# Kernel optimization log

Hardware: AMD Instinct MI355X
Metric: run time of the kernel (lower is better)

Reference implementation:

```python
import jax, jax.numpy as jnp
import numpy as np

D = 1024      # input_dim
H = 4096      # hidden_dim
E = 8         # expert_count
TOP_K = 2
N = 8192      # tokens
LN_EPS = 1e-5


def setup_inputs() -> dict:
    key = jax.random.key(0)
    ks = jax.random.split(key, 10)
    s_d = 1.0 / np.sqrt(D)
    s_h = 1.0 / np.sqrt(H)
    return {
        "x": jax.random.normal(ks[0], (N, D), dtype=jnp.float32),
        "ln_gamma": jnp.ones((D,), jnp.float32),
        "ln_beta": jnp.zeros((D,), jnp.float32),
        "conf_w": jax.random.uniform(ks[1], (D, 1), jnp.float32, -s_d, s_d),
        "conf_b": jnp.zeros((1,), jnp.float32),
        "router_w": jax.random.uniform(ks[2], (D, E), jnp.float32, -s_d, s_d),
        "router_b": jnp.zeros((E,), jnp.float32),
        "w1": jax.random.uniform(ks[3], (E, D, H), jnp.float32, -s_d, s_d),
        "b1": jax.random.uniform(ks[4], (E, H), jnp.float32, -s_d, s_d),
        "w2": jax.random.uniform(ks[5], (E, H, D), jnp.float32, -s_h, s_h),
        "b2": jax.random.uniform(ks[6], (E, D), jnp.float32, -s_h, s_h),
    }


def reference(x, ln_gamma, ln_beta, conf_w, conf_b, router_w, router_b, w1, b1, w2, b2):
    # LayerNorm (torch default eps=1e-5, affine)
    mu = jnp.mean(x, axis=-1, keepdims=True)
    var = jnp.mean(jnp.square(x - mu), axis=-1, keepdims=True)
    x_norm = (x - mu) * jax.lax.rsqrt(var + LN_EPS) * ln_gamma + ln_beta

    # layer-skip confidence head
    confidence = jax.nn.sigmoid(x_norm @ conf_w + conf_b)  # [N,1]

    # router: softmax -> top-k -> renormalize selected weights
    router_probs = jax.nn.softmax(x_norm @ router_w + router_b, axis=-1)  # [N,E]
    vals, indices = jax.lax.top_k(router_probs, TOP_K)                    # [N,K]
    vals = vals / jnp.sum(vals, axis=-1, keepdims=True)

    # scatter top-k weights into dense per-expert combine weights [N,E]
    combine_w = jnp.zeros((x.shape[0], E), x.dtype).at[
        jnp.arange(x.shape[0])[:, None], indices].add(vals)

    # dispatch/combine: loop over small fixed expert count (dense compute,
    # weighted by combine_w, mathematically identical to per-token dispatch)
    combined = jnp.zeros_like(x)
    for e in range(E):
        h = jax.nn.relu(x_norm @ w1[e] + b1[e])      # [N,H]
        combined = combined + combine_w[:, e:e + 1] * (h @ w2[e] + b2[e])

    output = x + combined
    return output, confidence, x
```

## Files before the change

kernel.cpp:

```cpp
#include <hip/hip_runtime.h>
#include <hip/hip_bf16.h>

#define N_TOK 8192
#define DIM   1024
#define HID   4096
#define NEXP  8
#define CSTR  64
#define RTMAX 136
#define HROWS 16896
#define EPS   264
#define NG1   (8 * 2 * RTMAX)

using bf16x8 = __attribute__((ext_vector_type(8))) short;
using f32x4  = __attribute__((ext_vector_type(4))) float;

__device__ __forceinline__ void gload_lds16(const void* g, void* l) {
  __builtin_amdgcn_global_load_lds(
      (const __attribute__((address_space(1))) unsigned int*)g,
      (__attribute__((address_space(3))) unsigned int*)l, 16, 0, 0);
}

__device__ __forceinline__ float wredsum(float v) {
#pragma unroll
  for (int off = 32; off > 0; off >>= 1) v += __shfl_xor(v, off, 64);
  return v;
}

__device__ __forceinline__ unsigned short f2bf(float f) {
  __hip_bfloat16 h = __float2bfloat16(f);
  return *reinterpret_cast<unsigned short*>(&h);
}
__device__ __forceinline__ float bf2f(unsigned short u) {
  return __uint_as_float((unsigned)u << 16);
}

__device__ __forceinline__ void transpose_body(
    const float* __restrict__ src, __hip_bfloat16* __restrict__ dst,
    int R, int C, int c0, int r0, float (*tile)[65]) {
  const int tid = threadIdx.x;
  const int tx = tid & 15, ty = tid >> 4;
#pragma unroll
  for (int k = 0; k < 4; k++) {
    const int row = ty + k * 16;
    const float4 v = *(const float4*)(src + (size_t)(r0 + row) * C + c0 + tx * 4);
    tile[row][tx * 4 + 0] = v.x; tile[row][tx * 4 + 1] = v.y;
    tile[row][tx * 4 + 2] = v.z; tile[row][tx * 4 + 3] = v.w;
  }
  __syncthreads();
#pragma unroll
  for (int k = 0; k < 4; k++) {
    const int orow = ty + k * 16;
    ushort4 st;
    st.x = f2bf(tile[tx * 4 + 0][orow]);
    st.y = f2bf(tile[tx * 4 + 1][orow]);
    st.z = f2bf(tile[tx * 4 + 2][orow]);
    st.w = f2bf(tile[tx * 4 + 3][orow]);
    *(ushort4*)((unsigned short*)dst + (size_t)(c0 + orow) * R + r0 + tx * 4) = st;
  }
}

__global__ __launch_bounds__(256) void setup_kernel(
    const float* __restrict__ x, const float* __restrict__ gamma, const float* __restrict__ beta,
    const float* __restrict__ conf_w, const float* __restrict__ conf_b,
    const float* __restrict__ rw, const float* __restrict__ rb,
    const float* __restrict__ w1,
    __hip_bfloat16* __restrict__ w1t,
    __hip_bfloat16* __restrict__ xn, float* __restrict__ out,
    int* __restrict__ counts, int* __restrict__ lists, float* __restrict__ wts,
    int2* __restrict__ idx) {
  __shared__ float tile[64][65];
  const int b = (int)blockIdx.x;
  if (b < 8192) {
    const int z = b >> 10, r = b & 1023;
    const int cx = r & 63, ry = r >> 6;
    transpose_body(w1 + (size_t)z * DIM * HID, w1t + (size_t)z * DIM * HID,
                   DIM, HID, cx * 64, ry * 64, tile);
    return;
  }
  const int t = (b - 8192) * 4 + ((int)threadIdx.x >> 6);
  const int lane = threadIdx.x & 63;
  const float* xr = x + (size_t)t * DIM;

  float4 xv[4];
#pragma unroll
  for (int q = 0; q < 4; q++) xv[q] = *(const float4*)(xr + q * 256 + lane * 4);

  float s = 0.f, s2 = 0.f;
#pragma unroll
  for (int q = 0; q < 4; q++) {
    s  += xv[q].x + xv[q].y + xv[q].z + xv[q].w;
    s2 += xv[q].x * xv[q].x + xv[q].y * xv[q].y + xv[q].z * xv[q].z + xv[q].w * xv[q].w;
  }
  s = wredsum(s); s2 = wredsum(s2);
  const float mu  = s * (1.f / DIM);
  const float inv = rsqrtf(s2 * (1.f / DIM) - mu * mu + 1e-5f);

  float p[9];
#pragma unroll
  for (int e = 0; e < 9; e++) p[e] = 0.f;

#pragma unroll
  for (int q = 0; q < 4; q++) {
    const int d0 = q * 256 + lane * 4;
    const float4 g4 = *(const float4*)(gamma + d0);
    const float4 b4 = *(const float4*)(beta + d0);
    float v0 = (xv[q].x - mu) * inv * g4.x + b4.x;
    float v1 = (xv[q].y - mu) * inv * g4.y + b4.y;
    float v2 = (xv[q].z - mu) * inv * g4.z + b4.z;
    float v3 = (xv[q].w - mu) * inv * g4.w + b4.w;

    ushort4 st; st.x = f2bf(v0); st.y = f2bf(v1); st.z = f2bf(v2); st.w = f2bf(v3);
    *(ushort4*)((unsigned short*)xn + (size_t)t * DIM + d0) = st;
    *(float4*)(out + (size_t)N_TOK * DIM + N_TOK + (size_t)t * DIM + d0) = xv[q];

    const float vv[4] = {v0, v1, v2, v3};
#pragma unroll
    for (int j = 0; j < 4; j++) {
      const int d = d0 + j;
      const float v = vv[j];
      p[8] += v * conf_w[d];
      const float4 r0 = *(const float4*)(rw + d * 8);
      const float4 r1 = *(const float4*)(rw + d * 8 + 4);
      p[0] += v * r0.x; p[1] += v * r0.y; p[2] += v * r0.z; p[3] += v * r0.w;
      p[4] += v * r1.x; p[5] += v * r1.y; p[6] += v * r1.z; p[7] += v * r1.w;
    }
  }
#pragma unroll
  for (int e = 0; e < 9; e++) p[e] = wredsum(p[e]);

  if (lane == 0) {
    float L[8];
#pragma unroll
    for (int e = 0; e < 8; e++) L[e] = p[e] + rb[e];
    const float cl = p[8] + conf_b[0];
    out[(size_t)N_TOK * DIM + t] = 1.f / (1.f + expf(-cl));

    float mx = L[0];
#pragma unroll
    for (int e = 1; e < 8; e++) mx = fmaxf(mx, L[e]);
    float pe[8];
#pragma unroll
    for (int e = 0; e < 8; e++) pe[e] = expf(L[e] - mx);
    int i0 = 0; float v0 = pe[0];
#pragma unroll
    for (int e = 1; e < 8; e++) if (pe[e] > v0) { v0 = pe[e]; i0 = e; }
    int i1 = -1; float v1 = -1.f;
#pragma unroll
    for (int e = 0; e < 8; e++) if (e != i0 && pe[e] > v1) { v1 = pe[e]; i1 = e; }
    const float wsum = v0 + v1;
    const float w0 = v0 / wsum, w1v = v1 / wsum;
    int p0 = atomicAdd(&counts[i0 * CSTR], 1);
    lists[i0 * N_TOK + p0] = t; wts[i0 * N_TOK + p0] = w0;
    int p1 = atomicAdd(&counts[i1 * CSTR], 1);
    lists[i1 * N_TOK + p1] = t; wts[i1 * N_TOK + p1] = w1v;
    idx[t] = make_int2((i0 << 13) | p0, (i1 << 13) | p1);
  }
}

__global__ void bases_kernel(const int* __restrict__ counts, int* __restrict__ bases,
                             int* __restrict__ meta) {
  if (threadIdx.x == 0) {
    int s = 0, r = 0;
#pragma unroll
    for (int e = 0; e < NEXP; e++) {
      bases[e] = s; meta[e] = r;
      const int c = counts[e * CSTR];
      s += c; r += (c + 127) >> 7;
    }
    meta[NEXP] = r;
  }
}


#define LGKM_SB(N)                                                            \
  asm volatile("s_waitcnt lgkmcnt(" #N ")" ::: "memory");                     \
  __builtin_amdgcn_sched_barrier(0);

#define MFMA_G(MI)                                                            \
  __builtin_amdgcn_s_setprio(1);                                              \
  _Pragma("unroll")                                                           \
  for (int n = 0; n < 4; n++)                                                 \
    acc[MI][n] = __builtin_amdgcn_mfma_f32_16x16x32_bf16(afr[MI], bfr[n], acc[MI][n], 0, 0, 0); \
  __builtin_amdgcn_s_setprio(0);

#define GEMM_CORE(NT)                                                                   \
  f32x4 acc[8][4] = {};                                                                 \
  stage(0, 0); stage(1, 24576);                                                         \
  for (int t = 0; t < (NT); ++t) {                                                      \
    const int pb = (t % 3) * 24576;                                                     \
    if (t + 1 < (NT)) { asm volatile("s_waitcnt vmcnt(6)" ::: "memory"); }              \
    else              { asm volatile("s_waitcnt vmcnt(0)" ::: "memory"); }              \
    __builtin_amdgcn_s_barrier();                                                       \
    if (t + 2 < (NT)) stage(t + 2, ((t + 2) % 3) * 24576);                              \
    const char* Ab = smem + pb + Abase;                                                 \
    const char* Bb = smem + pb + Bbase;                                                 \
    bf16x8 bfr[4], afr[8];                                                              \
    afr[0] = *(const bf16x8*)(Ab);                                                      \
    bfr[0] = *(const bf16x8*)(Bb);                                                      \
    bfr[1] = *(const bf16x8*)(Bb + 1024);                                               \
    __builtin_amdgcn_sched_barrier(0);                                                  \
    bfr[2] = *(const bf16x8*)(Bb + 2048);                                               \
    bfr[3] = *(const bf16x8*)(Bb + 3072);                                               \
    __builtin_amdgcn_sched_barrier(0);                                                  \
    _Pragma("unroll")                                                                   \
    for (int m = 1; m < 8; m++) {                                                       \
      afr[m] = *(const bf16x8*)(Ab + m * 1024);                                         \
      __builtin_amdgcn_sched_barrier(0);                                                \
    }                                                                                   \
    LGKM_SB(7) MFMA_G(0)                                                                \
    LGKM_SB(6) MFMA_G(1)                                                                \
    LGKM_SB(5) MFMA_G(2)                                                                \
    LGKM_SB(4) MFMA_G(3)                                                                \
    LGKM_SB(3) MFMA_G(4)                                                                \
    LGKM_SB(2) MFMA_G(5)                                                                \
    LGKM_SB(1) MFMA_G(6)                                                                \
    LGKM_SB(0) MFMA_G(7)                                                                \
  }

#define DECODE_TAIL()                                                         \
  if (rtg >= meta[NEXP]) return;                                              \
  int e = 0;                                                                  \
  _Pragma("unroll")                                                           \
  for (int k = 1; k < NEXP; k++) if (meta[k] <= rtg) e = k;                   \
  const int rt = rtg - meta[e];                                               \
  const int cnt = counts[e * CSTR];                                           \
  const int hbase = bases[e];

#define GEMM_COMMON()                                                         \
  const int tid = threadIdx.x;                     \
  const int l = tid & 63;                                                     \
  const int wc = tid >> 6;                                                    \
  const int lr = l & 15;                                                      \
  const int pchunk = (l >> 4) ^ ((lr >> 1) & 3);                              \
  const int Abase = lr * 64 + pchunk * 16;                                    \
  const int Bbase = 8192 + (wc * 64 + lr) * 64 + pchunk * 16;                 \
  const int srow = tid >> 2;                       \
  const int lc = (tid & 3) ^ ((srow >> 1) & 3);

#define EPILOGUE(DSTROW)                                                      \
  __builtin_amdgcn_s_barrier();                                               \
  {                                                                           \
    unsigned short* ep = (unsigned short*)smem;                               \
    _Pragma("unroll")                                                         \
    for (int n = 0; n < 4; n++) {                                             \
      const int col = wc * 64 + n * 16 + lr;                                  \
      _Pragma("unroll")                                                       \
      for (int m = 0; m < 8; m++) {                                           \
        f32x4 v = acc[m][n];                                                  \
        _Pragma("unroll")                                                     \
        for (int j = 0; j < 4; j++) {                                         \
          const int row = m * 16 + (l >> 4) * 4 + j;                          \
          ep[row * EPS + col] = f2bf(v[j]);                                   \
        }                                                                     \
      }                                                                       \
    }                                                                         \
    asm volatile("s_waitcnt lgkmcnt(0)" ::: "memory");                        \
    __builtin_amdgcn_s_barrier();                                             \
    const int g = tid >> 5, u = tid & 31;                                     \
    _Pragma("unroll")                                                         \
    for (int i = 0; i < 16; i++) {                                            \
      const int row = i * 8 + g;                                              \
      const int pos = rt * 128 + row;                                         \
      if (pos < cnt) {                                                        \
        bf16x8 vv = *(const bf16x8*)(ep + row * EPS + u * 8);                 \
        *(bf16x8*)(DSTROW + u * 8) = vv;                                      \
      }                                                                       \
    }                                                                         \
  }

__global__ __launch_bounds__(256, 2) void gemm1_kernel(
    const __hip_bfloat16* __restrict__ xn, const __hip_bfloat16* __restrict__ w1t_b,
    const float* __restrict__ b1, const int* __restrict__ lists,
    const int* __restrict__ counts, const int* __restrict__ bases,
    const int* __restrict__ meta, __hip_bfloat16* __restrict__ hbuf,
    const float* __restrict__ w2, __hip_bfloat16* __restrict__ w2t) {
  __shared__ char smem[73728];
  if ((int)blockIdx.x >= NG1) {
    const int bb = (int)blockIdx.x - NG1;
    const int z = bb >> 10, r = bb & 1023;
    const int cx = r & 15, ry = r >> 4;
    transpose_body(w2 + (size_t)z * HID * DIM, w2t + (size_t)z * HID * DIM,
                   HID, DIM, cx * 64, ry * 64, (float(*)[65])smem);
    return;
  }
  const int x_ = (int)blockIdx.x & 7;
  const int q_ = (int)blockIdx.x >> 3;
  const int rtg = q_ >> 1;
  const int panel = x_ * 2 + (q_ & 1);
  DECODE_TAIL()
  const int ct = panel;
  const int* list = lists + e * N_TOK;
  const __hip_bfloat16* w1t = w1t_b + (size_t)e * DIM * HID;
  GEMM_COMMON()

  const int ap0 = rt * 128 + srow, ap1 = ap0 + 64;
  const int tok0 = list[ap0 < cnt ? ap0 : 0];
  const int tok1 = list[ap1 < cnt ? ap1 : 0];
  const unsigned short* srcA0 = (const unsigned short*)xn + (size_t)tok0 * DIM + lc * 8;
  const unsigned short* srcA1 = (const unsigned short*)xn + (size_t)tok1 * DIM + lc * 8;
  const unsigned short* srcB0 = (const unsigned short*)w1t + (size_t)(ct * 256 + srow) * DIM + lc * 8;
  const unsigned short* srcB1 = (const unsigned short*)w1t + (size_t)(ct * 256 + 64 + srow) * DIM + lc * 8;
  const unsigned short* srcB2 = (const unsigned short*)w1t + (size_t)(ct * 256 + 128 + srow) * DIM + lc * 8;
  const unsigned short* srcB3 = (const unsigned short*)w1t + (size_t)(ct * 256 + 192 + srow) * DIM + lc * 8;

  auto stage = [&](int tt, int lbase) {
    gload_lds16(srcA0 + tt * 32, smem + lbase + tid * 16);
    gload_lds16(srcA1 + tt * 32, smem + lbase + 4096 + tid * 16);
    gload_lds16(srcB0 + tt * 32, smem + lbase + 8192 + tid * 16);
    gload_lds16(srcB1 + tt * 32, smem + lbase + 12288 + tid * 16);
    gload_lds16(srcB2 + tt * 32, smem + lbase + 16384 + tid * 16);
    gload_lds16(srcB3 + tt * 32, smem + lbase + 20480 + tid * 16);
  };

  GEMM_CORE(DIM / 32)

  const float bv[4] = {
    b1[e * HID + ct * 256 + wc * 64 + 0 * 16 + lr],
    b1[e * HID + ct * 256 + wc * 64 + 1 * 16 + lr],
    b1[e * HID + ct * 256 + wc * 64 + 2 * 16 + lr],
    b1[e * HID + ct * 256 + wc * 64 + 3 * 16 + lr]};
#pragma unroll
  for (int n = 0; n < 4; n++)
#pragma unroll
    for (int m = 0; m < 8; m++)
#pragma unroll
      for (int j = 0; j < 4; j++) acc[m][n][j] = fmaxf(acc[m][n][j] + bv[n], 0.f);
  EPILOGUE((unsigned short*)hbuf + (size_t)(hbase + pos) * HID + ct * 256)
}

__global__ __launch_bounds__(256, 2) void gemm2_kernel(
    const __hip_bfloat16* __restrict__ hbuf, const __hip_bfloat16* __restrict__ w2t_b,
    const int* __restrict__ counts, const int* __restrict__ bases,
    const int* __restrict__ meta, __hip_bfloat16* __restrict__ ybuf, const int SK) {
  __shared__ char smem[73728];
  int panel, rtg;
  if (SK == 2) {
    const int x_ = (int)blockIdx.x & 7;
    const int q_ = (int)blockIdx.x >> 3;
    rtg = (q_ >> 2) * 4 + (x_ >> 1);
    panel = (x_ & 1) * 4 + (q_ & 3);
  } else {
    panel = (int)blockIdx.x / RTMAX;
    rtg = (int)blockIdx.x - panel * RTMAX;
  }
  DECODE_TAIL()
  const int ct = panel & 3;
  const int ksp = panel >> 2;
  const int kbase = ksp * (HID / SK);
  const __hip_bfloat16* w2t = w2t_b + (size_t)e * DIM * HID;
  GEMM_COMMON()

  const unsigned short* srcA0 = (const unsigned short*)hbuf +
      (size_t)(hbase + rt * 128 + srow) * HID + kbase + lc * 8;
  const unsigned short* srcA1 = (const unsigned short*)hbuf +
      (size_t)(hbase + rt * 128 + 64 + srow) * HID + kbase + lc * 8;
  const unsigned short* srcB0 = (const unsigned short*)w2t +
      (size_t)(ct * 256 + srow) * HID + kbase + lc * 8;
  const unsigned short* srcB1 = (const unsigned short*)w2t +
      (size_t)(ct * 256 + 64 + srow) * HID + kbase + lc * 8;
  const unsigned short* srcB2 = (const unsigned short*)w2t +
      (size_t)(ct * 256 + 128 + srow) * HID + kbase + lc * 8;
  const unsigned short* srcB3 = (const unsigned short*)w2t +
      (size_t)(ct * 256 + 192 + srow) * HID + kbase + lc * 8;

  auto stage = [&](int tt, int lbase) {
    gload_lds16(srcA0 + tt * 32, smem + lbase + tid * 16);
    gload_lds16(srcA1 + tt * 32, smem + lbase + 4096 + tid * 16);
    gload_lds16(srcB0 + tt * 32, smem + lbase + 8192 + tid * 16);
    gload_lds16(srcB1 + tt * 32, smem + lbase + 12288 + tid * 16);
    gload_lds16(srcB2 + tt * 32, smem + lbase + 16384 + tid * 16);
    gload_lds16(srcB3 + tt * 32, smem + lbase + 20480 + tid * 16);
  };

  const int nk = (HID / 32) / SK;
  GEMM_CORE(nk)

  EPILOGUE((unsigned short*)ybuf + ((size_t)ksp * HROWS + hbase + pos) * DIM + ct * 256)
}

__global__ __launch_bounds__(256) void combine_kernel(
    const float* __restrict__ x, const __hip_bfloat16* __restrict__ ybuf,
    const float* __restrict__ b2, const int2* __restrict__ idx,
    const float* __restrict__ wv, const int* __restrict__ bases,
    float* __restrict__ out, const int SK) {
  const int t = blockIdx.x * 4 + (threadIdx.x >> 6);
  const int lane = threadIdx.x & 63;
  const int2 iv = idx[t];
  const int e0 = iv.x >> 13, p0 = iv.x & (N_TOK - 1);
  const int e1 = iv.y >> 13, p1 = iv.y & (N_TOK - 1);
  const float w0 = wv[iv.x], w1 = wv[iv.y];
  const int r0 = bases[e0] + p0;
  const int r1 = bases[e1] + p1;
#pragma unroll
  for (int q = 0; q < 4; q++) {
    const int d0 = q * 256 + lane * 4;
    float4 o = *(const float4*)(x + (size_t)t * DIM + d0);
    float y0x = 0.f, y0y = 0.f, y0z = 0.f, y0w = 0.f;
    float y1x = 0.f, y1y = 0.f, y1z = 0.f, y1w = 0.f;
    for (int s = 0; s < SK; s++) {
      const ushort4 a = *(const ushort4*)((const unsigned short*)ybuf +
                          ((size_t)s * HROWS + r0) * DIM + d0);
      const ushort4 b = *(const ushort4*)((const unsigned short*)ybuf +
                          ((size_t)s * HROWS + r1) * DIM + d0);
      y0x += bf2f(a.x); y0y += bf2f(a.y); y0z += bf2f(a.z); y0w += bf2f(a.w);
      y1x += bf2f(b.x); y1y += bf2f(b.y); y1z += bf2f(b.z); y1w += bf2f(b.w);
    }
    const float4 bb0 = *(const float4*)(b2 + e0 * DIM + d0);
    const float4 bb1 = *(const float4*)(b2 + e1 * DIM + d0);
    o.x += w0 * (y0x + bb0.x) + w1 * (y1x + bb1.x);
    o.y += w0 * (y0y + bb0.y) + w1 * (y1y + bb1.y);
    o.z += w0 * (y0z + bb0.z) + w1 * (y1z + bb1.z);
    o.w += w0 * (y0w + bb0.w) + w1 * (y1w + bb1.w);
    *(float4*)(out + (size_t)t * DIM + d0) = o;
  }
}

extern "C" void kernel_launch(void* const* d_in, const int* in_sizes, int n_in,
                              void* d_out, int out_size, void* d_ws, size_t ws_size,
                              hipStream_t stream) {
  (void)in_sizes; (void)n_in; (void)out_size;
  const float* x      = (const float*)d_in[0];
  const float* gamma  = (const float*)d_in[1];
  const float* beta   = (const float*)d_in[2];
  const float* conf_w = (const float*)d_in[3];
  const float* conf_b = (const float*)d_in[4];
  const float* rw     = (const float*)d_in[5];
  const float* rb     = (const float*)d_in[6];
  const float* w1     = (const float*)d_in[7];
  const float* b1     = (const float*)d_in[8];
  const float* w2     = (const float*)d_in[9];
  const float* b2     = (const float*)d_in[10];
  float* out = (float*)d_out;

  char* w = (char*)d_ws;
  auto alloc = [&](size_t bytes) { char* p = w; w += (bytes + 255) & ~255ULL; return p; };

  __hip_bfloat16* xn = (__hip_bfloat16*)alloc((size_t)N_TOK * DIM * 2);
  int*   lists  = (int*)alloc((size_t)NEXP * N_TOK * 4);
  float* wtsb   = (float*)alloc((size_t)NEXP * N_TOK * 4);
  int*   counts = (int*)alloc(NEXP * CSTR * 4);
  int*   bases  = (int*)alloc(256);
  int*   meta   = (int*)alloc(256);
  int2*  idx    = (int2*)alloc((size_t)N_TOK * 8);

  const size_t hbufA = (size_t)HROWS * HID * 2;
  const size_t wtA   = (size_t)NEXP * DIM * HID * 2;
  __hip_bfloat16* hbuf = (__hip_bfloat16*)alloc(hbufA);
  __hip_bfloat16* w1t  = (__hip_bfloat16*)alloc(wtA);
  __hip_bfloat16* w2t  = (__hip_bfloat16*)alloc(wtA);
  const size_t used = (size_t)(w - (char*)d_ws);
  const size_t ybuf1 = (size_t)HROWS * DIM * 2;

  int SK;
  __hip_bfloat16* ybuf;
  if (ws_size >= used + 2 * ybuf1 + 4096) {
    SK = 2; ybuf = (__hip_bfloat16*)alloc(2 * ybuf1);
  } else {
    SK = 1; ybuf = w1t;
  }
  const int g2grid = (SK == 2) ? 8 * RTMAX : 4 * RTMAX;

  hipMemsetAsync(counts, 0, NEXP * CSTR * 4, stream);
  setup_kernel<<<8192 + N_TOK / 4, 256, 0, stream>>>(
      x, gamma, beta, conf_w, conf_b, rw, rb, w1, w1t,
      xn, out, counts, lists, wtsb, idx);
  bases_kernel<<<1, 64, 0, stream>>>(counts, bases, meta);
  gemm1_kernel<<<NG1 + 8192, 256, 0, stream>>>(xn, w1t, b1, lists, counts, bases, meta,
                                               hbuf, w2, w2t);
  gemm2_kernel<<<g2grid, 256, 0, stream>>>(hbuf, w2t, counts, bases, meta, ybuf, SK);
  combine_kernel<<<N_TOK / 4, 256, 0, stream>>>(x, ybuf, b2, idx, wtsb, bases, out, SK);
}
```

Baseline: 459.4 us.

## Load weight B-fragments directly into registers with one-step prefetch, bypassing LDS

Both expert GEMM kernels now stage only the activation (A) tiles through LDS. Each wave loads its own weight (B) fragments straight from global memory into registers, one K-step ahead. B tiles were never shared across waves, so this removes the LDS writes and reads for B and shrinks the triple-buffered LDS footprint to a third. The cost is that global-load latency for B is hidden by only one iteration of MFMA work. The register copy at the end of each loop forces a wait on those loads, and in-order vmcnt may also make it wait on the A prefetch, which can serialize memory and compute. It also raises register pressure.

```diff
diff --git a/kernel.cpp b/kernel.cpp
--- a/kernel.cpp
+++ b/kernel.cpp
@@ -180,30 +180,27 @@
   __builtin_amdgcn_s_setprio(1);                                              \
   _Pragma("unroll")                                                           \
   for (int n = 0; n < 4; n++)                                                 \
-    acc[MI][n] = __builtin_amdgcn_mfma_f32_16x16x32_bf16(afr[MI], bfr[n], acc[MI][n], 0, 0, 0); \
+    acc[MI][n] = __builtin_amdgcn_mfma_f32_16x16x32_bf16(afr[MI], bcur[n], acc[MI][n], 0, 0, 0); \
   __builtin_amdgcn_s_setprio(0);
 
 #define GEMM_CORE(NT)                                                                   \
   f32x4 acc[8][4] = {};                                                                 \
-  stage(0, 0); stage(1, 24576);                                                         \
+  bf16x8 bcur[4], bnxt[4];                                                              \
+  stageA(0, 0); stageA(1, 8192);                                                        \
+  loadB(0, bcur);                                                                       \
   for (int t = 0; t < (NT); ++t) {                                                      \
-    const int pb = (t % 3) * 24576;                                                     \
+    const int pb = (t % 3) * 8192;                                                      \
     if (t + 1 < (NT)) { asm volatile("s_waitcnt vmcnt(6)" ::: "memory"); }              \
-    else              { asm volatile("s_waitcnt vmcnt(0)" ::: "memory"); }              \
+    else              { asm volatile("s_waitcnt vmcnt(4)" ::: "memory"); }              \
     __builtin_amdgcn_s_barrier();                                                       \
-    if (t + 2 < (NT)) stage(t + 2, ((t + 2) % 3) * 24576);                              \
+    if (t + 1 < (NT)) loadB(t + 1, bnxt);                                               \
+    __builtin_amdgcn_sched_barrier(0);                                                  \
+    if (t + 2 < (NT)) stageA(t + 2, ((t + 2) % 3) * 8192);                              \
+    __builtin_amdgcn_sched_barrier(0);                                                  \
     const char* Ab = smem + pb + Abase;                                                 \
-    const char* Bb = smem + pb + Bbase;                                                 \
-    bf16x8 bfr[4], afr[8];                                                              \
-    afr[0] = *(const bf16x8*)(Ab);                                                      \
-    bfr[0] = *(const bf16x8*)(Bb);                                                      \
-    bfr[1] = *(const bf16x8*)(Bb + 1024);                                               \
-    __builtin_amdgcn_sched_barrier(0);                                                  \
-    bfr[2] = *(const bf16x8*)(Bb + 2048);                                               \
-    bfr[3] = *(const bf16x8*)(Bb + 3072);                                               \
-    __builtin_amdgcn_sched_barrier(0);                                                  \
+    bf16x8 afr[8];                                                                      \
     _Pragma("unroll")                                                                   \
-    for (int m = 1; m < 8; m++) {                                                       \
+    for (int m = 0; m < 8; m++) {                                                       \
       afr[m] = *(const bf16x8*)(Ab + m * 1024);                                         \
       __builtin_amdgcn_sched_barrier(0);                                                \
     }                                                                                   \
@@ -215,6 +212,9 @@
     LGKM_SB(2) MFMA_G(5)                                                                \
     LGKM_SB(1) MFMA_G(6)                                                                \
     LGKM_SB(0) MFMA_G(7)                                                                \
+    __builtin_amdgcn_sched_barrier(0);                                                  \
+    _Pragma("unroll")                                                                   \
+    for (int n = 0; n < 4; n++) bcur[n] = bnxt[n];                                      \
   }
 
 #define DECODE_TAIL()                                                         \
@@ -233,7 +233,6 @@
   const int lr = l & 15;                                                      \
   const int pchunk = (l >> 4) ^ ((lr >> 1) & 3);                              \
   const int Abase = lr * 64 + pchunk * 16;                                    \
-  const int Bbase = 8192 + (wc * 64 + lr) * 64 + pchunk * 16;                 \
   const int srow = tid >> 2;                       \
   const int lc = (tid & 3) ^ ((srow >> 1) & 3);
 
@@ -298,18 +297,17 @@
   const int tok1 = list[ap1 < cnt ? ap1 : 0];
   const unsigned short* srcA0 = (const unsigned short*)xn + (size_t)tok0 * DIM + lc * 8;
   const unsigned short* srcA1 = (const unsigned short*)xn + (size_t)tok1 * DIM + lc * 8;
-  const unsigned short* srcB0 = (const unsigned short*)w1t + (size_t)(ct * 256 + srow) * DIM + lc * 8;
-  const unsigned short* srcB1 = (const unsigned short*)w1t + (size_t)(ct * 256 + 64 + srow) * DIM + lc * 8;
-  const unsigned short* srcB2 = (const unsigned short*)w1t + (size_t)(ct * 256 + 128 + srow) * DIM + lc * 8;
-  const unsigned short* srcB3 = (const unsigned short*)w1t + (size_t)(ct * 256 + 192 + srow) * DIM + lc * 8;
-
-  auto stage = [&](int tt, int lbase) {
+  auto stageA = [&](int tt, int lbase) {
     gload_lds16(srcA0 + tt * 32, smem + lbase + tid * 16);
     gload_lds16(srcA1 + tt * 32, smem + lbase + 4096 + tid * 16);
-    gload_lds16(srcB0 + tt * 32, smem + lbase + 8192 + tid * 16);
-    gload_lds16(srcB1 + tt * 32, smem + lbase + 12288 + tid * 16);
-    gload_lds16(srcB2 + tt * 32, smem + lbase + 16384 + tid * 16);
-    gload_lds16(srcB3 + tt * 32, smem + lbase + 20480 + tid * 16);
+  };
+
+  const unsigned short* bptr = (const unsigned short*)w1t +
+      (size_t)(ct * 256 + wc * 64 + lr) * DIM + (l >> 4) * 8;
+  auto loadB = [&](int tt, bf16x8* dst) {
+#pragma unroll
+    for (int n = 0; n < 4; n++)
+      dst[n] = *(const bf16x8*)(bptr + (size_t)n * 16 * DIM + tt * 32);
   };
 
   GEMM_CORE(DIM / 32)
@@ -354,22 +352,17 @@
       (size_t)(hbase + rt * 128 + srow) * HID + kbase + lc * 8;
   const unsigned short* srcA1 = (const unsigned short*)hbuf +
       (size_t)(hbase + rt * 128 + 64 + srow) * HID + kbase + lc * 8;
-  const unsigned short* srcB0 = (const unsigned short*)w2t +
-      (size_t)(ct * 256 + srow) * HID + kbase + lc * 8;
-  const unsigned short* srcB1 = (const unsigned short*)w2t +
-      (size_t)(ct * 256 + 64 + srow) * HID + kbase + lc * 8;
-  const unsigned short* srcB2 = (const unsigned short*)w2t +
-      (size_t)(ct * 256 + 128 + srow) * HID + kbase + lc * 8;
-  const unsigned short* srcB3 = (const unsigned short*)w2t +
-      (size_t)(ct * 256 + 192 + srow) * HID + kbase + lc * 8;
-
-  auto stage = [&](int tt, int lbase) {
+  auto stageA = [&](int tt, int lbase) {
     gload_lds16(srcA0 + tt * 32, smem + lbase + tid * 16);
     gload_lds16(srcA1 + tt * 32, smem + lbase + 4096 + tid * 16);
-    gload_lds16(srcB0 + tt * 32, smem + lbase + 8192 + tid * 16);
-    gload_lds16(srcB1 + tt * 32, smem + lbase + 12288 + tid * 16);
-    gload_lds16(srcB2 + tt * 32, smem + lbase + 16384 + tid * 16);
-    gload_lds16(srcB3 + tt * 32, smem + lbase + 20480 + tid * 16);
+  };
+
+  const unsigned short* bptr = (const unsigned short*)w2t +
+      (size_t)(ct * 256 + wc * 64 + lr) * HID + kbase + (l >> 4) * 8;
+  auto loadB = [&](int tt, bf16x8* dst) {
+#pragma unroll
+    for (int n = 0; n < 4; n++)
+      dst[n] = *(const bf16x8*)(bptr + (size_t)n * 16 * HID + tt * 32);
   };
 
   const int nk = (HID / 32) / SK;
```

After: 576.4 us. 1.25x slower.
